# Kernel optimization log

Hardware: AMD Instinct MI355X
Metric: run time of the kernel (lower is better)

Reference implementation:

```python
import jax, jax.numpy as jnp
import numpy as np

B, T, N1, K = 128, 512, 512, 8   # batch, steps, n_customers+1, knn_k
CAPACITY = 50.0
NEG_INF = -1e9


def setup_inputs() -> dict:
    key = jax.random.key(0)
    k0, k1, k2, k3, k4, k5 = jax.random.split(key, 6)
    psi_prime = jax.random.normal(k0, (B, N1, 2), dtype=jnp.float32)
    demands = jax.random.uniform(k1, (B, N1), dtype=jnp.float32) * 9.0 + 1.0
    demands = demands.at[:, 0].set(0.0)  # depot has zero demand
    actions = jax.random.randint(k2, (B, T), 0, N1, dtype=jnp.int32)
    knn_indices = jax.random.randint(k3, (B, N1, K), 0, N1, dtype=jnp.int32)
    Wq_w = jax.random.normal(k4, (2, 4), dtype=jnp.float32) * 0.5
    Wq_b = jax.random.normal(k5, (2,), dtype=jnp.float32) * 0.1
    lambda_param = jnp.float32(0.1)
    return {"psi_prime": psi_prime, "demands": demands, "Wq_w": Wq_w,
            "Wq_b": Wq_b, "lambda_param": lambda_param,
            "actions": actions, "knn_indices": knn_indices}


def _rollout_states(demands, actions):
    """Reconstruct the T per-step states (cur, used, vis) BEFORE each action."""
    mb, Tn = actions.shape
    n1 = demands.shape[1]
    batch = jnp.arange(mb)

    def step(carry, act_t):
        cur, used, vis = carry
        out = (cur, used, vis)  # record state before applying act_t
        at_depot = act_t == 0
        dem_t = jnp.take_along_axis(demands, act_t[:, None], axis=1)[:, 0]
        used_n = jnp.where(at_depot, 0.0, used + dem_t)
        vis_n = vis.at[batch, act_t].set(True)
        vis_n = vis_n.at[:, 0].set(False)
        return (act_t, used_n, vis_n), out

    init = (jnp.zeros((mb,), jnp.int32), jnp.zeros((mb,), jnp.float32),
            jnp.zeros((mb, n1), dtype=bool))
    _, (all_cur, all_used, all_vis) = jax.lax.scan(step, init, actions.T)
    # scan stacks over leading T axis -> move batch first
    return all_cur.T, all_used.T, jnp.transpose(all_vis, (1, 0, 2))


def _evaluate(psi_prime, demands, Wq_w, Wq_b, lambda_param, actions, knn_indices):
    mb, Tn = actions.shape
    n_cust = psi_prime.shape[1] - 1

    all_cur, all_used, all_vis = _rollout_states(demands, actions)  # [B,T],[B,T],[B,T,N1]

    remaining = CAPACITY - all_used                      # [B,T]
    cap_norm = remaining / max(CAPACITY, 1e-8)
    exceeds = demands[:, None, :] > remaining[:, :, None]  # [B,T,N1]
    mask = all_vis | exceeds
    mask = mask.at[:, :, 0].set(False)
    at_depot = all_cur == 0                               # [B,T]
    has_cust = jnp.any(~mask[:, :, 1:], axis=-1)
    mask = mask.at[:, :, 0].set(at_depot & has_cust)

    psi_curr = jnp.take_along_axis(psi_prime, all_cur[:, :, None], axis=1)  # [B,T,2]
    psi_curr = jnp.where(at_depot[:, :, None], 0.0, psi_curr)
    t_norm = jnp.arange(Tn, dtype=jnp.float32) / max(n_cust, 1)
    t_norm = jnp.broadcast_to(t_norm[None, :], (mb, Tn))
    ctx = jnp.concatenate([psi_curr, cap_norm[:, :, None], t_norm[:, :, None]], axis=-1)  # [B,T,4]

    query = ctx @ Wq_w.T + Wq_b                           # [B,T,2]
    context_scores = jnp.einsum('btd,bnd->btn', query, psi_prime)  # [B,T,N1]

    # kNN interference: per-node dot with its k nearest neighbours, summed
    neigh = psi_prime[jnp.arange(mb)[:, None, None], knn_indices]  # [B,N1,K,2]
    interf = jnp.einsum('bnd,bnkd->bn', psi_prime, neigh)          # [B,N1]

    scores = context_scores + lambda_param * interf[:, None, :]
    scores = jnp.where(mask, NEG_INF, scores)
    log_probs = jax.nn.log_softmax(scores, axis=-1)                # [B,T,N1]

    lp_new = jnp.take_along_axis(log_probs, actions[:, :, None], axis=2)[:, :, 0]  # [B,T]
    ent = -jnp.sum(jnp.exp(log_probs) * log_probs, axis=-1)        # [B,T]
    entropy = ent.mean(axis=1)                                     # [B]
    return lp_new, entropy


def reference(psi_prime, demands, Wq_w, Wq_b, lambda_param, actions, knn_indices):
    return _evaluate(psi_prime, demands, Wq_w, Wq_b, lambda_param, actions, knn_indices)
```

## Files before the change

kernel.cpp:

```cpp
#include <hip/hip_runtime.h>
#include <hip/hip_bf16.h>

#define B_  128
#define T_  512
#define N1_ 512
#define K_  8
#define CAPf 50.0f
#define NEG_INF_F (-1000000000.0f)

__device__ __forceinline__ int   fi(float x) { return __float_as_int(x); }
__device__ __forceinline__ float uf(int x)   { return __int_as_float(x); }

__device__ __forceinline__ float wave_sum64(float x) {
    x += uf(__builtin_amdgcn_update_dpp(0, fi(x), 0x111, 0xF, 0xF, true));
    x += uf(__builtin_amdgcn_update_dpp(0, fi(x), 0x112, 0xF, 0xF, true));
    x += uf(__builtin_amdgcn_update_dpp(0, fi(x), 0x114, 0xF, 0xF, true));
    x += uf(__builtin_amdgcn_update_dpp(0, fi(x), 0x118, 0xF, 0xF, true));
    x += uf(__builtin_amdgcn_update_dpp(0, fi(x), 0x142, 0xA, 0xF, true));
    x += uf(__builtin_amdgcn_update_dpp(0, fi(x), 0x143, 0xC, 0xF, true));
    return uf(__builtin_amdgcn_readlane(fi(x), 63));
}
__device__ __forceinline__ float wave_max64_pos(float x) {
    x = fmaxf(x, uf(__builtin_amdgcn_update_dpp(0, fi(x), 0x111, 0xF, 0xF, true)));
    x = fmaxf(x, uf(__builtin_amdgcn_update_dpp(0, fi(x), 0x112, 0xF, 0xF, true)));
    x = fmaxf(x, uf(__builtin_amdgcn_update_dpp(0, fi(x), 0x114, 0xF, 0xF, true)));
    x = fmaxf(x, uf(__builtin_amdgcn_update_dpp(0, fi(x), 0x118, 0xF, 0xF, true)));
    x = fmaxf(x, uf(__builtin_amdgcn_update_dpp(0, fi(x), 0x142, 0xA, 0xF, true)));
    x = fmaxf(x, uf(__builtin_amdgcn_update_dpp(0, fi(x), 0x143, 0xC, 0xF, true)));
    return uf(__builtin_amdgcn_readlane(fi(x), 63));
}

__global__ __launch_bounds__(256) void prep_kernel(
    const float* __restrict__ psi,
    const float* __restrict__ demands,
    const float* __restrict__ lambda_p,
    const int*   __restrict__ actions,
    const int*   __restrict__ knn,
    float4* __restrict__ ws_pk,
    int*    __restrict__ ws_fv,
    float*  __restrict__ ws_used)
{
    __shared__ float2 psi_l[N1_];
    __shared__ float  dem_l[N1_];
    __shared__ int    fv_l[N1_];
    __shared__ int    act_l[T_];
    __shared__ float2 md_l[T_];

    const int b   = blockIdx.x;
    const int tid = threadIdx.x;

    const float2* psi2 = (const float2*)psi;
    for (int i = tid; i < N1_; i += 256) {
        psi_l[i] = psi2[b * N1_ + i];
        dem_l[i] = demands[b * N1_ + i];
        fv_l[i]  = 0x7fffffff;
    }
    for (int t = tid; t < T_; t += 256) act_l[t] = actions[b * T_ + t];
    __syncthreads();

    for (int t = tid; t < T_; t += 256) {
        int a = act_l[t];
        atomicMin(&fv_l[a], t);
        float d = dem_l[a];
        md_l[t] = (a == 0) ? make_float2(0.0f, 0.0f) : make_float2(1.0f, d);
    }
    __syncthreads();

    if (tid == 0) {
        float u = 0.0f;
        #pragma unroll 8
        for (int t = 0; t < T_; ++t) {
            ws_used[b * T_ + t] = u;
            float2 md = md_l[t];
            u = fmaf(md.x, u, md.y);
        }
    } else if (tid >= 64) {
        const float lam = *lambda_p;
        for (int n = tid - 64; n < N1_; n += 192) {
            float2 p = psi_l[n];
            const int4* kk = (const int4*)(knn + ((size_t)b * N1_ + n) * K_);
            int4 k0 = kk[0], k1 = kk[1];
            int ks[8] = {k0.x, k0.y, k0.z, k0.w, k1.x, k1.y, k1.z, k1.w};
            float acc = 0.0f;
            #pragma unroll
            for (int k = 0; k < 8; ++k) {
                float2 q = psi_l[ks[k]];
                acc = fmaf(p.x, q.x, acc);
                acc = fmaf(p.y, q.y, acc);
            }
            ws_pk[b * N1_ + n] = make_float4(p.x, p.y, lam * acc, dem_l[n]);
        }
    }
    __syncthreads();
    for (int n = tid; n < N1_; n += 256) ws_fv[b * N1_ + n] = fv_l[n];
}

__global__ __launch_bounds__(256, 8) void main_kernel(
    const float*  __restrict__ Wq_w,
    const float*  __restrict__ Wq_b,
    const int*    __restrict__ actions,
    const float4* __restrict__ ws_pk,
    const int*    __restrict__ ws_fv,
    const float*  __restrict__ ws_used,
    float* __restrict__ out_lp,
    float* __restrict__ out_ent)
{
    __shared__ float used_s[32];
    __shared__ int   act_s[33];
    __shared__ float went[4];

    const int bid    = blockIdx.x;
    const int b      = bid >> 4;
    const int chunk  = bid & 15;
    const int t_base = chunk * 32;
    const int tid    = threadIdx.x;
    const int wave   = tid >> 6;
    const int lane   = tid & 63;

    if (tid < 32) used_s[tid] = ws_used[b * T_ + t_base + tid];
    if (tid < 33) {
        int tt = t_base - 1 + tid;
        act_s[tid] = (tt < 0) ? 0 : actions[b * T_ + tt];
    }

    float4 pk[8];
    int    fvr[8];
    #pragma unroll
    for (int j = 0; j < 8; ++j) {
        pk[j]  = ws_pk[b * N1_ + j * 64 + lane];
        fvr[j] = ws_fv[b * N1_ + j * 64 + lane];
    }
    const float W00 = Wq_w[0], W01 = Wq_w[1], W02 = Wq_w[2], W03 = Wq_w[3];
    const float W10 = Wq_w[4], W11 = Wq_w[5], W12 = Wq_w[6], W13 = Wq_w[7];
    const float bq0 = Wq_b[0], bq1 = Wq_b[1];
    __syncthreads();

    float ent_acc = 0.0f;

    #pragma unroll 1
    for (int r = 0; r < 8; ++r) {
        const int i   = wave * 8 + r;
        const int t   = t_base + i;
        const int cur = (t == 0) ? 0 : act_s[i];
        const int a   = act_s[i + 1];
        const float rem = CAPf - used_s[i];
        const float cap = rem * (1.0f / CAPf);
        const float tn  = (float)t * (1.0f / 511.0f);
        const bool  at_depot = (cur == 0);

        float pcx = 0.0f, pcy = 0.0f;
        if (!at_depot) {
            float4 pc = ws_pk[b * N1_ + cur];
            pcx = pc.x; pcy = pc.y;
        }

        const float q0 = fmaf(pcx, W00, fmaf(pcy, W01, fmaf(cap, W02, fmaf(tn, W03, bq0))));
        const float q1 = fmaf(pcx, W10, fmaf(pcy, W11, fmaf(cap, W12, fmaf(tn, W13, bq1))));

        float s[8];
        bool avail = false;
        #pragma unroll
        for (int j = 0; j < 8; ++j) {
            const int n = j * 64 + lane;
            float sc = fmaf(q0, pk[j].x, fmaf(q1, pk[j].y, pk[j].z));
            if (n != 0) {
                bool m = (fvr[j] < t) | (pk[j].w > rem);
                avail |= !m;
                sc = m ? NEG_INF_F : sc;
            }
            s[j] = sc;
        }

        const bool has_cust = __any((int)avail);
        if (lane == 0 && at_depot && has_cust) s[0] = NEG_INF_F;

        float pre = s[0];
        #pragma unroll
        for (int j = 1; j < 8; ++j) pre = fmaxf(pre, s[j]);
        const float mx = wave_max64_pos(pre + 1024.0f) - 1024.0f;

        float S1 = 0.0f, S2 = 0.0f;
        #pragma unroll
        for (int j = 0; j < 8; ++j) {
            float e = __expf(s[j] - mx);
            S1 += e;
            S2 = fmaf(e, s[j], S2);
        }
        S1 = wave_sum64(S1);
        S2 = wave_sum64(S2);
        const float lse = mx + __logf(S1);

        const int ja = a >> 6;
        float sv = s[0];
        sv = (ja == 1) ? s[1] : sv;
        sv = (ja == 2) ? s[2] : sv;
        sv = (ja == 3) ? s[3] : sv;
        sv = (ja == 4) ? s[4] : sv;
        sv = (ja == 5) ? s[5] : sv;
        sv = (ja == 6) ? s[6] : sv;
        sv = (ja == 7) ? s[7] : sv;
        const float s_a = uf(__builtin_amdgcn_readlane(fi(sv), a & 63));

        if (lane == 0) out_lp[b * T_ + t] = s_a - lse;
        ent_acc += lse - __fdividef(S2, S1);
    }

    if (lane == 0) went[wave] = ent_acc;
    __syncthreads();
    if (tid == 0) {
        float s = (went[0] + went[1]) + (went[2] + went[3]);
        atomicAdd(&out_ent[b], s * (1.0f / 512.0f));
    }
}

extern "C" void kernel_launch(void* const* d_in, const int* in_sizes, int n_in,
                              void* d_out, int out_size, void* d_ws, size_t ws_size,
                              hipStream_t stream) {
    const float* psi      = (const float*)d_in[0];
    const float* demands  = (const float*)d_in[1];
    const float* Wq_w     = (const float*)d_in[2];
    const float* Wq_b     = (const float*)d_in[3];
    const float* lam      = (const float*)d_in[4];
    const int*   actions  = (const int*)d_in[5];
    const int*   knn      = (const int*)d_in[6];

    float* out_lp  = (float*)d_out;
    float* out_ent = out_lp + (size_t)B_ * T_;

    float4* ws_pk  = (float4*)d_ws;
    int*    ws_fv  = (int*)  ((char*)d_ws + (size_t)B_ * N1_ * 16);
    float*  ws_used= (float*)((char*)d_ws + (size_t)B_ * N1_ * 20);

    prep_kernel<<<B_, 256, 0, stream>>>(psi, demands, lam, actions, knn,
                                        ws_pk, ws_fv, ws_used);
    main_kernel<<<B_ * 16, 256, 0, stream>>>(Wq_w, Wq_b, actions,
                                             ws_pk, ws_fv, ws_used,
                                             out_lp, out_ent);
}
```

Before: 99.18 us.

## Process two timesteps per iteration and compute softmax in base-2 domain

Scores are pre-scaled by log2(e), folded into lambda and the query, so the softmax can use the native exp2/log2 instructions directly, with a single ln2 rescale at the output. The per-wave loop now handles two timesteps per iteration so the independent reductions can interleave and hide DPP and transcendental latency. Launch bounds drop from 8 to 4 waves per SIMD to leave room for the extra registers. The risks are lower occupancy and small numerical differences from the change of base.

Result: no change. 99.61 us (+0.4%).

```diff
diff --git a/kernel.cpp b/kernel.cpp
--- a/kernel.cpp
+++ b/kernel.cpp
@@ -7,6 +7,9 @@
 #define K_  8
 #define CAPf 50.0f
 #define NEG_INF_F (-1000000000.0f)
+#define NEG_INF_L2 (-1442695040.0f)
+#define L2E  1.44269504088896341f
+#define LN2  0.69314718055994531f
 
 __device__ __forceinline__ int   fi(float x) { return __float_as_int(x); }
 __device__ __forceinline__ float uf(int x)   { return __int_as_float(x); }
@@ -75,7 +78,7 @@
             u = fmaf(md.x, u, md.y);
         }
     } else if (tid >= 64) {
-        const float lam = *lambda_p;
+        const float lam = (*lambda_p) * L2E;
         for (int n = tid - 64; n < N1_; n += 192) {
             float2 p = psi_l[n];
             const int4* kk = (const int4*)(knn + ((size_t)b * N1_ + n) * K_);
@@ -95,7 +98,7 @@
     for (int n = tid; n < N1_; n += 256) ws_fv[b * N1_ + n] = fv_l[n];
 }
 
-__global__ __launch_bounds__(256, 8) void main_kernel(
+__global__ __launch_bounds__(256, 4) void main_kernel(
     const float*  __restrict__ Wq_w,
     const float*  __restrict__ Wq_b,
     const int*    __restrict__ actions,
@@ -138,78 +141,102 @@
     float ent_acc = 0.0f;
 
     #pragma unroll 1
-    for (int r = 0; r < 8; ++r) {
-        const int i   = wave * 8 + r;
-        const int t   = t_base + i;
-        const int cur = (t == 0) ? 0 : act_s[i];
-        const int a   = act_s[i + 1];
-        const float rem = CAPf - used_s[i];
-        const float cap = rem * (1.0f / CAPf);
-        const float tn  = (float)t * (1.0f / 511.0f);
-        const bool  at_depot = (cur == 0);
-
-        float pcx = 0.0f, pcy = 0.0f;
-        if (!at_depot) {
-            float4 pc = ws_pk[b * N1_ + cur];
-            pcx = pc.x; pcy = pc.y;
-        }
-
-        const float q0 = fmaf(pcx, W00, fmaf(pcy, W01, fmaf(cap, W02, fmaf(tn, W03, bq0))));
-        const float q1 = fmaf(pcx, W10, fmaf(pcy, W11, fmaf(cap, W12, fmaf(tn, W13, bq1))));
-
-        float s[8];
-        bool avail = false;
+    for (int rr = 0; rr < 4; ++rr) {
+        const int iA = wave * 8 + rr * 2;
+        const int iB = iA + 1;
+        const int tA = t_base + iA;
+        const int tB = t_base + iB;
+        const int curA = (tA == 0) ? 0 : act_s[iA];
+        const int curB = act_s[iB];
+        const int aA = act_s[iA + 1];
+        const int aB = act_s[iB + 1];
+        const float remA = CAPf - used_s[iA];
+        const float remB = CAPf - used_s[iB];
+        const bool depA = (curA == 0);
+        const bool depB = (curB == 0);
+
+        float4 pcA = ws_pk[b * N1_ + curA];
+        float4 pcB = ws_pk[b * N1_ + curB];
+        const float pcxA = depA ? 0.0f : pcA.x, pcyA = depA ? 0.0f : pcA.y;
+        const float pcxB = depB ? 0.0f : pcB.x, pcyB = depB ? 0.0f : pcB.y;
+
+        const float capA = remA * (1.0f / CAPf), capB = remB * (1.0f / CAPf);
+        const float tnA = (float)tA * (1.0f / 511.0f);
+        const float tnB = (float)tB * (1.0f / 511.0f);
+
+        const float q0A = fmaf(pcxA, W00, fmaf(pcyA, W01, fmaf(capA, W02, fmaf(tnA, W03, bq0)))) * L2E;
+        const float q1A = fmaf(pcxA, W10, fmaf(pcyA, W11, fmaf(capA, W12, fmaf(tnA, W13, bq1)))) * L2E;
+        const float q0B = fmaf(pcxB, W00, fmaf(pcyB, W01, fmaf(capB, W02, fmaf(tnB, W03, bq0)))) * L2E;
+        const float q1B = fmaf(pcxB, W10, fmaf(pcyB, W11, fmaf(capB, W12, fmaf(tnB, W13, bq1)))) * L2E;
+
+        float sA[8], sB[8];
+        bool avA = false, avB = false;
         #pragma unroll
         for (int j = 0; j < 8; ++j) {
             const int n = j * 64 + lane;
-            float sc = fmaf(q0, pk[j].x, fmaf(q1, pk[j].y, pk[j].z));
+            float scA = fmaf(q0A, pk[j].x, fmaf(q1A, pk[j].y, pk[j].z));
+            float scB = fmaf(q0B, pk[j].x, fmaf(q1B, pk[j].y, pk[j].z));
             if (n != 0) {
-                bool m = (fvr[j] < t) | (pk[j].w > rem);
-                avail |= !m;
-                sc = m ? NEG_INF_F : sc;
+                bool mA = (fvr[j] < tA) | (pk[j].w > remA);
+                bool mB = (fvr[j] < tB) | (pk[j].w > remB);
+                avA |= !mA;  avB |= !mB;
+                scA = mA ? NEG_INF_L2 : scA;
+                scB = mB ? NEG_INF_L2 : scB;
             }
-            s[j] = sc;
-        }
-
-        const bool has_cust = __any((int)avail);
-        if (lane == 0 && at_depot && has_cust) s[0] = NEG_INF_F;
-
-        float pre = s[0];
-        #pragma unroll
-        for (int j = 1; j < 8; ++j) pre = fmaxf(pre, s[j]);
-        const float mx = wave_max64_pos(pre + 1024.0f) - 1024.0f;
-
-        float S1 = 0.0f, S2 = 0.0f;
+            sA[j] = scA;  sB[j] = scB;
+        }
+
+        const bool hasA = __any((int)avA);
+        const bool hasB = __any((int)avB);
+        if (lane == 0 && depA && hasA) sA[0] = NEG_INF_L2;
+        if (lane == 0 && depB && hasB) sB[0] = NEG_INF_L2;
+
+        float preA = fmaxf(fmaxf(fmaxf(sA[0], sA[1]), fmaxf(sA[2], sA[3])),
+                           fmaxf(fmaxf(sA[4], sA[5]), fmaxf(sA[6], sA[7])));
+        float preB = fmaxf(fmaxf(fmaxf(sB[0], sB[1]), fmaxf(sB[2], sB[3])),
+                           fmaxf(fmaxf(sB[4], sB[5]), fmaxf(sB[6], sB[7])));
+        const float mxA = wave_max64_pos(preA + 2048.0f) - 2048.0f;
+        const float mxB = wave_max64_pos(preB + 2048.0f) - 2048.0f;
+
+        float S1A = 0.0f, S2A = 0.0f, S1B = 0.0f, S2B = 0.0f;
         #pragma unroll
         for (int j = 0; j < 8; ++j) {
-            float e = __expf(s[j] - mx);
-            S1 += e;
-            S2 = fmaf(e, s[j], S2);
-        }
-        S1 = wave_sum64(S1);
-        S2 = wave_sum64(S2);
-        const float lse = mx + __logf(S1);
-
-        const int ja = a >> 6;
-        float sv = s[0];
-        sv = (ja == 1) ? s[1] : sv;
-        sv = (ja == 2) ? s[2] : sv;
-        sv = (ja == 3) ? s[3] : sv;
-        sv = (ja == 4) ? s[4] : sv;
-        sv = (ja == 5) ? s[5] : sv;
-        sv = (ja == 6) ? s[6] : sv;
-        sv = (ja == 7) ? s[7] : sv;
-        const float s_a = uf(__builtin_amdgcn_readlane(fi(sv), a & 63));
-
-        if (lane == 0) out_lp[b * T_ + t] = s_a - lse;
-        ent_acc += lse - __fdividef(S2, S1);
+            float eA = __builtin_amdgcn_exp2f(sA[j] - mxA);
+            float eB = __builtin_amdgcn_exp2f(sB[j] - mxB);
+            S1A += eA;  S2A = fmaf(eA, sA[j], S2A);
+            S1B += eB;  S2B = fmaf(eB, sB[j], S2B);
+        }
+        S1A = wave_sum64(S1A);  S2A = wave_sum64(S2A);
+        S1B = wave_sum64(S1B);  S2B = wave_sum64(S2B);
+
+        const float lgA = __builtin_amdgcn_logf(S1A);
+        const float lgB = __builtin_amdgcn_logf(S1B);
+
+        const int jaA = aA >> 6, jaB = aB >> 6;
+        float svA = sA[0], svB = sB[0];
+        svA = (jaA == 1) ? sA[1] : svA;  svB = (jaB == 1) ? sB[1] : svB;
+        svA = (jaA == 2) ? sA[2] : svA;  svB = (jaB == 2) ? sB[2] : svB;
+        svA = (jaA == 3) ? sA[3] : svA;  svB = (jaB == 3) ? sB[3] : svB;
+        svA = (jaA == 4) ? sA[4] : svA;  svB = (jaB == 4) ? sB[4] : svB;
+        svA = (jaA == 5) ? sA[5] : svA;  svB = (jaB == 5) ? sB[5] : svB;
+        svA = (jaA == 6) ? sA[6] : svA;  svB = (jaB == 6) ? sB[6] : svB;
+        svA = (jaA == 7) ? sA[7] : svA;  svB = (jaB == 7) ? sB[7] : svB;
+        const float s_aA = uf(__builtin_amdgcn_readlane(fi(svA), aA & 63));
+        const float s_aB = uf(__builtin_amdgcn_readlane(fi(svB), aB & 63));
+
+        if (lane == 0) {
+            out_lp[b * T_ + tA] = LN2 * ((s_aA - mxA) - lgA);
+            out_lp[b * T_ + tB] = LN2 * ((s_aB - mxB) - lgB);
+        }
+        ent_acc += ((mxA + lgA) - __fdividef(S2A, S1A))
+                 + ((mxB + lgB) - __fdividef(S2B, S1B));
     }
 
     if (lane == 0) went[wave] = ent_acc;
     __syncthreads();
     if (tid == 0) {
         float s = (went[0] + went[1]) + (went[2] + went[3]);
-        atomicAdd(&out_ent[b], s * (1.0f / 512.0f));
+        atomicAdd(&out_ent[b], s * (LN2 / 512.0f));
     }
 }
 
```
